# Optimization experiments

Measured on AMD Instinct MI355X. Metric: run time of the kernel, lower is better.

## Reference

```python
import jax, jax.numpy as jnp
import numpy as np

NUM_CLASSES = 2
TOP_K = 1500
CONF_THRESH = 0.01
NMS_THRESH = 0.2
VAR0, VAR1 = 0.1, 0.2  # cfg['variance']


def setup_inputs() -> dict:
    key = jax.random.key(0)
    k1, k2, k3 = jax.random.split(key, 3)
    B, P = 32, 76800
    loc_data = jax.random.normal(k1, (B, P, 4), jnp.float32)
    conf_data = jax.random.uniform(k2, (B * P, NUM_CLASSES), jnp.float32)
    prior_data = jax.random.uniform(k3, (P, 4), jnp.float32)
    return {"loc_data": loc_data, "conf_data": conf_data, "prior_data": prior_data}


def _decode(loc, priors):
    # loc, priors: [P,4]; SSD box decode with variances
    cxcy = priors[:, :2] + loc[:, :2] * VAR0 * priors[:, 2:]
    wh = priors[:, 2:] * jnp.exp(loc[:, 2:] * VAR1)
    x1y1 = cxcy - wh * 0.5
    return jnp.concatenate([x1y1, x1y1 + wh], axis=-1)  # [P,4] (x1,y1,x2,y2)


def _nms_per_class(scores, boxes):
    # scores: [P], boxes: [P,4] -> [TOP_K,5] packed (score,x1,y1,x2,y2)
    s = jnp.where(scores > CONF_THRESH, scores, -jnp.inf)
    sk, idx = jax.lax.top_k(s, TOP_K)  # torch nms keeps only top_k candidates
    bk = boxes[idx]
    x1, y1, x2, y2 = bk[:, 0], bk[:, 1], bk[:, 2], bk[:, 3]
    area = (x2 - x1) * (y2 - y1)
    iota = jnp.arange(TOP_K)

    def step(active, i):
        # greedy NMS over score-descending candidates
        xx1 = jnp.maximum(x1, x1[i]); yy1 = jnp.maximum(y1, y1[i])
        xx2 = jnp.minimum(x2, x2[i]); yy2 = jnp.minimum(y2, y2[i])
        inter = jnp.maximum(xx2 - xx1, 0.0) * jnp.maximum(yy2 - yy1, 0.0)
        iou = inter / (area + area[i] - inter)
        kept = active[i]
        suppress = (iou > NMS_THRESH) & (iota != i)
        active = jnp.where(kept, active & ~suppress, active)
        return active, kept

    _, keep = jax.lax.scan(step, sk > -jnp.inf, iota)
    rows = jnp.where(keep[:, None], jnp.concatenate([sk[:, None], bk], axis=1), 0.0)
    # pack kept rows at the front (score-descending order), zeros after
    rank = jnp.cumsum(keep) - 1
    dest = jnp.where(keep, rank, TOP_K)  # dump non-kept into scratch slot
    return jnp.zeros((TOP_K + 1, 5), bk.dtype).at[dest].set(rows)[:TOP_K]


def reference(loc_data, conf_data, prior_data):
    B, P, _ = loc_data.shape
    conf = conf_data.reshape(B, P, NUM_CLASSES)
    decoded = jax.vmap(_decode, in_axes=(0, None))(loc_data, prior_data)  # [B,P,4]
    outs = []
    for cl in range(1, NUM_CLASSES):  # background class 0 stays zero
        outs.append(jax.vmap(_nms_per_class)(conf[:, :, cl], decoded))
    bg = jnp.zeros((B, 1, TOP_K, 5), decoded.dtype)
    return jnp.concatenate([bg, jnp.stack(outs, axis=1)], axis=1)  # [B,C,TOP_K,5]
```

## Files before the change

### kernel.cpp

```cpp
#include <hip/hip_runtime.h>
#include <stdint.h>

typedef unsigned long long u64;
typedef unsigned int u32;

#define NUM_B 32
#define NUM_P 76800
#define TOPK 1500
#define NBINS 2048
#define CAP 2048
#define NWORDS 24
#define NCHUNK 6
#define HSLICES 16
#define HCHUNK (NUM_P / HSLICES)
#define PB 1984
#define SCAP 512

__device__ __forceinline__ u32 fbits(float f) { return __float_as_uint(f); }
__device__ __forceinline__ int binOf(float s) {
    int b = (int)(s * (float)NBINS);
    return (b > NBINS - 1) ? NBINS - 1 : b;
}
__device__ __forceinline__ u64 readlane64(u64 v, int l) {
    u32 lo = (u32)__builtin_amdgcn_readlane((int)(u32)(v & 0xffffffffu), l);
    u32 hi = (u32)__builtin_amdgcn_readlane((int)(u32)(v >> 32), l);
    return ((u64)hi << 32) | lo;
}

__global__ __launch_bounds__(256) void hist_kernel(const float4* __restrict__ conf4,
                                                   u32* __restrict__ hist,
                                                   u32* __restrict__ bpos,
                                                   u64* __restrict__ skey,
                                                   u32* __restrict__ scnt) {
    int c = blockIdx.x, b = blockIdx.y, tid = threadIdx.x;
    if (tid < NBINS / HSLICES) bpos[(size_t)b * NBINS + c * (NBINS / HSLICES) + tid] = 0;
    __shared__ u32 h[NBINS];
    __shared__ u64 stg[SCAP];
    __shared__ u32 sc_s;
    if (tid == 0) sc_s = 0;
    for (int i = tid; i < NBINS; i += 256) h[i] = 0;
    __syncthreads();
    const float4* base = conf4 + (size_t)b * (NUM_P / 2) + (size_t)c * (HCHUNK / 2);
    int pbase = c * HCHUNK;
    for (int i = tid; i < HCHUNK / 2; i += 256) {
        float4 v = base[i];
        int p0 = pbase + i * 2;
        if (v.y > 0.01f) {
            int bn = binOf(v.y);
            atomicAdd(&h[bn], 1u);
            if (bn >= PB) {
                u32 s = atomicAdd(&sc_s, 1u);
                if (s < SCAP) stg[s] = ((u64)fbits(v.y) << 32) | (u32)(~p0);
            }
        }
        if (v.w > 0.01f) {
            int bn = binOf(v.w);
            atomicAdd(&h[bn], 1u);
            if (bn >= PB) {
                u32 s = atomicAdd(&sc_s, 1u);
                if (s < SCAP) stg[s] = ((u64)fbits(v.w) << 32) | (u32)(~(p0 + 1));
            }
        }
    }
    __syncthreads();
    u32* outp = hist + ((size_t)b * HSLICES + c) * NBINS;
    for (int i = tid; i < NBINS; i += 256) outp[i] = h[i];
    u32 n = sc_s;
    if (tid == 0) scnt[b * HSLICES + c] = n;
    u64* sk = skey + (size_t)(b * HSLICES + c) * SCAP;
    u32 nn = (n < (u32)SCAP) ? n : (u32)SCAP;
    for (u32 i = tid; i < nn; i += 256) sk[i] = stg[i];
}

__global__ void thresh_kernel(const u32* __restrict__ hist, int* __restrict__ tbin,
                              u32* __restrict__ binbase, u32* __restrict__ bincnt,
                              u32* __restrict__ ntotal) {
    int b = blockIdx.x;
    int tid = threadIdx.x;
    int lane = tid & 63, wid = tid >> 6;
    const u32* hb = hist + (size_t)b * HSLICES * NBINS;
    __shared__ u32 wsum[4];
    __shared__ int s_min[NBINS / 256];
    if (tid < NBINS / 256) s_min[tid] = 256;
    __syncthreads();
    u32 total = 0;
    for (int c = 0; c < NBINS / 256; ++c) {
        int bin = NBINS - 1 - (c * 256 + tid);
        u32 v = 0;
#pragma unroll
        for (int s = 0; s < HSLICES; ++s) v += hb[(size_t)s * NBINS + bin];
        u32 x = v;
#pragma unroll
        for (int off = 1; off < 64; off <<= 1) {
            u32 y = __shfl_up(x, off, 64);
            if (lane >= off) x += y;
        }
        if (lane == 63) wsum[wid] = x;
        __syncthreads();
        u32 woff = 0;
        for (int w2 = 0; w2 < wid; ++w2) woff += wsum[w2];
        u32 csum = wsum[0] + wsum[1] + wsum[2] + wsum[3];
        u32 incl = woff + x;
        u32 cum = total + incl;
        binbase[(size_t)b * NBINS + bin] = cum - v;
        bincnt [(size_t)b * NBINS + bin] = v;
        if (cum >= TOPK) atomicMin(&s_min[c], tid);
        __syncthreads();
        int sm = s_min[c];
        if (sm < 256) {
            if (tid == sm) { tbin[b] = bin; ntotal[b] = cum; }
            return;
        }
        total += csum;
    }
    if (tid == 0) { tbin[b] = 0; ntotal[b] = total; }
}

__global__ __launch_bounds__(256) void compact_kernel(
    const float4* __restrict__ conf4, const int* __restrict__ tbin,
    const u32* __restrict__ binbase, u32* __restrict__ bpos,
    u64* __restrict__ keys, const u64* __restrict__ skey,
    const u32* __restrict__ scnt) {
    int b = blockIdx.y;
    int tid = threadIdx.x;
    int tb = tbin[b];
    if (tb >= PB) {
        bool ovf = false;
#pragma unroll
        for (int s = 0; s < HSLICES; ++s) ovf |= (scnt[b * HSLICES + s] > (u32)SCAP);
        if (!ovf) {
            if (blockIdx.x >= HSLICES) return;
            int sl = blockIdx.x;
            u32 cnt = scnt[b * HSLICES + sl];
            const u64* sk = skey + (size_t)(b * HSLICES + sl) * SCAP;
            for (u32 i = tid; i < cnt; i += 256) {
                u64 key = sk[i];
                float sc = __uint_as_float((u32)(key >> 32));
                int bn = binOf(sc);
                if (bn >= tb) {
                    u32 slot = atomicAdd(&bpos[(size_t)b * NBINS + bn], 1u);
                    u32 pos = binbase[(size_t)b * NBINS + bn] + slot;
                    if (pos < CAP) keys[(size_t)b * CAP + pos] = key;
                }
            }
            return;
        }
    }
    int f4 = blockIdx.x * 256 + tid;
    float4 c = conf4[(size_t)b * (NUM_P / 2) + f4];
    int p0 = f4 * 2, p1 = p0 + 1;
    int b0 = binOf(c.y);
    if (c.y > 0.01f && b0 >= tb) {
        u32 slot = atomicAdd(&bpos[(size_t)b * NBINS + b0], 1u);
        u32 pos = binbase[(size_t)b * NBINS + b0] + slot;
        if (pos < CAP) keys[(size_t)b * CAP + pos] = ((u64)fbits(c.y) << 32) | (u32)(~p0);
    }
    int b1 = binOf(c.w);
    if (c.w > 0.01f && b1 >= tb) {
        u32 slot = atomicAdd(&bpos[(size_t)b * NBINS + b1], 1u);
        u32 pos = binbase[(size_t)b * NBINS + b1] + slot;
        if (pos < CAP) keys[(size_t)b * CAP + pos] = ((u64)fbits(c.w) << 32) | (u32)(~p1);
    }
}

__global__ __launch_bounds__(256) void rank_decode_kernel(
    const u64* __restrict__ keys, const u32* __restrict__ binbase,
    const u32* __restrict__ bincnt, const u32* __restrict__ ntotal,
    const float* __restrict__ loc, const float* __restrict__ prior,
    float* __restrict__ sscore, float* __restrict__ sbox) {
#pragma clang fp contract(off)
    int b = blockIdx.y;
    int g = blockIdx.x * 256 + threadIdx.x;
    int n = (int)min(ntotal[b], (u32)CAP);
    if (g >= n) return;
    const u64* kb = keys + (size_t)b * CAP;
    u64 mykey = kb[g];
    float sc = __uint_as_float((u32)(mykey >> 32));
    int bn = binOf(sc);
    u32 start = binbase[(size_t)b * NBINS + bn];
    u32 end = start + bincnt[(size_t)b * NBINS + bn];
    if (end > (u32)n) end = (u32)n;
    u32 rank = start;
#pragma unroll 4
    for (u32 j = start; j < end; ++j) rank += (kb[j] > mykey) ? 1u : 0u;

    if (rank < TOPK) {
        u32 pidx = ~(u32)mykey;
        const float* lp = &loc[((size_t)b * NUM_P + pidx) * 4];
        const float* pp = &prior[(size_t)pidx * 4];
        float lx = lp[0], ly = lp[1], lw = lp[2], lh = lp[3];
        float pcx = pp[0], pcy = pp[1], pw = pp[2], ph = pp[3];
        float cx = pcx + (lx * 0.1f) * pw;
        float cy = pcy + (ly * 0.1f) * ph;
        float w  = pw * expf(lw * 0.2f);
        float h  = ph * expf(lh * 0.2f);
        float x1 = cx - w * 0.5f;
        float y1 = cy - h * 0.5f;
        float x2 = x1 + w;
        float y2 = y1 + h;
        sscore[(size_t)b * TOPK + rank] = sc;
        float* bx = &sbox[((size_t)b * TOPK + rank) * 4];
        bx[0] = x1; bx[1] = y1; bx[2] = x2; bx[3] = y2;
    }
}

__global__ __launch_bounds__(256) void mask_kernel(
    const float* __restrict__ sbox, u64* __restrict__ mask) {
#pragma clang fp contract(off)
    int w = blockIdx.x, c = blockIdx.y, b = blockIdx.z, tid = threadIdx.x;
    int i = c * 256 + tid;
    if ((w * 64 + 63) <= (c * 256)) return;
    __shared__ float4 cbox[64];
    __shared__ float car[64];
    if (tid < 64) {
        int j = w * 64 + tid;
        float4 bx = make_float4(0.f, 0.f, 0.f, 0.f);
        if (j < TOPK) bx = ((const float4*)sbox)[(size_t)b * TOPK + j];
        cbox[tid] = bx;
        car[tid] = (bx.z - bx.x) * (bx.w - bx.y);
    }
    __syncthreads();
    if (i < TOPK && (w * 64 + 63) > i) {
        const double MID = 0.5 * ((double)__uint_as_float(0x3E4CCCCDu) +
                                  (double)__uint_as_float(0x3E4CCCCEu));
        const float4 bx = ((const float4*)sbox)[(size_t)b * TOPK + i];
        float x1i = bx.x, y1i = bx.y, x2i = bx.z, y2i = bx.w;
        float ai = (x2i - x1i) * (y2i - y1i);
        u64 jmask = (i < w * 64) ? ~0ULL : (~0ULL << (i - w * 64 + 1));
        u64 m = 0;
        for (int j2 = 0; j2 < 64; ++j2) {
            float4 cb = cbox[j2];
            float xx1 = fmaxf(cb.x, x1i);
            float yy1 = fmaxf(cb.y, y1i);
            float xx2 = fminf(cb.z, x2i);
            float yy2 = fminf(cb.w, y2i);
            float iw = fmaxf(xx2 - xx1, 0.0f);
            float ih = fmaxf(yy2 - yy1, 0.0f);
            float inter = iw * ih;
            float denom = (car[j2] + ai) - inter;
            if ((double)inter >= MID * (double)denom) m |= (1ULL << j2);
        }
        m &= jmask;
        mask[((size_t)b * NWORDS + w) * TOPK + i] = m;
    }
}

__global__ __launch_bounds__(256) void sweep_kernel(
    const u64* __restrict__ mask, const float* __restrict__ sscore,
    const float* __restrict__ sbox, float* __restrict__ out) {
    int b = blockIdx.x, tid = threadIdx.x;
    int lane = tid & 63, wid = tid >> 6;

    const u64* mbase = mask + (size_t)b * NWORDS * TOPK;

    __shared__ u64 rowbuf[3][NWORDS][65];
    __shared__ u64 aw[NWORDS];
    __shared__ u32 pfx[NWORDS + 1];

    u64 act = 0;
    u64 sv[8];
    if (wid == 0) {
        for (int c = 0; c < NWORDS; ++c) {
            int r = c * 64 + lane;
            bool v = (r < TOPK) && (sscore[(size_t)b * TOPK + r] > 0.0f);
            u64 m = __ballot(v);
            if (lane == c) act = m;
        }
    } else {
        int w0 = (wid - 1) * 8;
#pragma unroll
        for (int t = 0; t < 2; ++t) {
            u64 tmp[8];
#pragma unroll
            for (int k = 0; k < 8; ++k)
                tmp[k] = (w0 + k >= t) ? mbase[(size_t)(w0 + k) * TOPK + t * 64 + lane] : 0ULL;
#pragma unroll
            for (int k = 0; k < 8; ++k)
                rowbuf[t][w0 + k][lane] = tmp[k];
        }
        {
            int rr = 2 * 64 + lane;
#pragma unroll
            for (int k = 0; k < 8; ++k)
                sv[k] = (w0 + k >= 2) ? mbase[(size_t)(w0 + k) * TOPK + rr] : 0ULL;
        }
    }
    __syncthreads();

    for (int T = 0; T < NWORDS; ++T) {
        if (wid == 0) {
            u64 dreg = rowbuf[T % 3][T][lane];
            u64 actw = readlane64(act, T);
            u64 kept = 0, rem = actw;
            while (rem) {
                int i2 = __ffsll(rem) - 1;
                kept |= (1ULL << i2);
                rem &= rem - 1;
                rem &= ~readlane64(dreg, i2);
            }
            if (lane == T) act = kept;
            if (lane > T && lane < NWORDS) {
                const u64* rb = rowbuf[T % 3][lane];
                if (__popcll(kept) > 4) {
                    u64 acc = 0;
#pragma unroll 16
                    for (int j = 0; j < 64; ++j) {
                        u64 sel = (u64)0 - ((kept >> j) & 1ULL);
                        acc |= rb[j] & sel;
                    }
                    act &= ~acc;
                } else {
                    u64 kb = kept;
                    while (kb) {
                        int r = __ffsll(kb) - 1;
                        kb &= kb - 1;
                        act &= ~rb[r];
                    }
                }
            }
        } else {
            int tw = T + 2;
            if (tw < NWORDS) {
                int w0 = (wid - 1) * 8;
#pragma unroll
                for (int k = 0; k < 8; ++k)
                    rowbuf[tw % 3][w0 + k][lane] = sv[k];
                int tn = T + 3;
                if (tn < NWORDS) {
                    int rr = tn * 64 + lane;
                    bool vr = rr < TOPK;
#pragma unroll
                    for (int k = 0; k < 8; ++k)
                        sv[k] = (vr && (w0 + k >= tn))
                                    ? mbase[(size_t)(w0 + k) * TOPK + rr] : 0ULL;
                }
            }
        }
        __syncthreads();
    }

    if (wid == 0 && lane < NWORDS) aw[lane] = act;
    {
        float4* pz = (float4*)(out + (size_t)b * 2 * TOPK * 5);
        float4 z4 = make_float4(0.f, 0.f, 0.f, 0.f);
        for (int t = tid; t < (2 * TOPK * 5) / 4; t += 256) pz[t] = z4;
    }
    __syncthreads();
    if (tid == 0) {
        u32 acc = 0;
        for (int wd = 0; wd < NWORDS; ++wd) { pfx[wd] = acc; acc += (u32)__popcll(aw[wd]); }
        pfx[NWORDS] = acc;
    }
    __syncthreads();
    for (int r = tid; r < TOPK; r += 256) {
        int wd = r >> 6;
        u64 word = aw[wd];
        if ((word >> (r & 63)) & 1ULL) {
            u32 rank = pfx[wd] + (u32)__popcll(word & ((1ULL << (r & 63)) - 1ULL));
            float sc = sscore[(size_t)b * TOPK + r];
            float4 bx = ((const float4*)sbox)[(size_t)b * TOPK + r];
            size_t base_o = (((size_t)b * 2 + 1) * TOPK + (size_t)rank) * 5;
            out[base_o + 0] = sc;
            out[base_o + 1] = bx.x;
            out[base_o + 2] = bx.y;
            out[base_o + 3] = bx.z;
            out[base_o + 4] = bx.w;
        }
    }
}

extern "C" void kernel_launch(void* const* d_in, const int* in_sizes, int n_in,
                              void* d_out, int out_size, void* d_ws, size_t ws_size,
                              hipStream_t stream) {
    const float* loc   = (const float*)d_in[0];
    const float* conf  = (const float*)d_in[1];
    const float* prior = (const float*)d_in[2];
    float* out = (float*)d_out;
    char* ws = (char*)d_ws;

    u64* mask_buf = (u64*)(ws + 0);
    u32* hist     = (u32*)(ws + 0);
    u32* binbase  = (u32*)(ws + 4194304);
    u32* bincnt   = (u32*)(ws + 4456448);
    u32* bpos     = (u32*)(ws + 4718592);
    u64* keys     = (u64*)(ws + 4980736);
    int* tbin     = (int*)(ws + 5505024);
    u32* ntotal   = (u32*)(ws + 5505152);
    u64* skey     = (u64*)(ws + 5505280);
    u32* scnt     = (u32*)(ws + 7602432);
    float* sscore = (float*)(ws + 9216000);
    float* sbox   = (float*)(ws + 9408000);

    hist_kernel<<<dim3(HSLICES, 32), 256, 0, stream>>>((const float4*)conf, hist, bpos,
                                                       skey, scnt);
    thresh_kernel<<<32, 256, 0, stream>>>(hist, tbin, binbase, bincnt, ntotal);
    compact_kernel<<<dim3(150, 32), 256, 0, stream>>>((const float4*)conf, tbin, binbase,
                                                      bpos, keys, skey, scnt);
    rank_decode_kernel<<<dim3(CAP / 256, 32), 256, 0, stream>>>(keys, binbase, bincnt,
                                                                ntotal, loc, prior,
                                                                sscore, sbox);
    mask_kernel<<<dim3(NWORDS, NCHUNK, 32), 256, 0, stream>>>(sbox, mask_buf);
    sweep_kernel<<<32, 256, 0, stream>>>(mask_buf, sscore, sbox, out);
}
```

Measured before the change: 182.5 us.

## Preload all upper-triangle mask tiles to LDS and drop per-step barriers in sweep

The sweep kernel used to stream mask tiles through a triple-buffered LDS ring, with a block barrier on each of the 24 word steps. It now loads every upper-triangular tile (276 pairs) into shared memory once, keeps the diagonal rows in wave-0 registers, and runs the whole greedy sweep inside wave 0 with no barriers. The other waves zero the output in parallel. The suppression OR-loop now skips 16-bit groups of kept with no bits set. The trade-off is about 143 KB of LDS per block, which limits occupancy, plus a serialized upfront load with no overlap. Wave 0 also uses 24 extra 64-bit registers.

```diff
diff --git a/kernel.cpp b/kernel.cpp
--- a/kernel.cpp
+++ b/kernel.cpp
@@ -15,6 +15,7 @@
 #define HCHUNK (NUM_P / HSLICES)
 #define PB 1984
 #define SCAP 512
+#define NPAIR 276
 
 __device__ __forceinline__ u32 fbits(float f) { return __float_as_uint(f); }
 __device__ __forceinline__ int binOf(float s) {
@@ -253,13 +254,17 @@
 
     const u64* mbase = mask + (size_t)b * NWORDS * TOPK;
 
-    __shared__ u64 rowbuf[3][NWORDS][65];
+    __shared__ u64 tb[NPAIR * 65];
     __shared__ u64 aw[NWORDS];
     __shared__ u32 pfx[NWORDS + 1];
 
     u64 act = 0;
-    u64 sv[8];
+    u64 dr[NWORDS];
+
     if (wid == 0) {
+#pragma unroll
+        for (int t = 0; t < NWORDS; ++t)
+            dr[t] = mbase[(size_t)t * TOPK + t * 64 + lane];
         for (int c = 0; c < NWORDS; ++c) {
             int r = c * 64 + lane;
             bool v = (r < TOPK) && (sscore[(size_t)b * TOPK + r] > 0.0f);
@@ -267,29 +272,18 @@
             if (lane == c) act = m;
         }
     } else {
-        int w0 = (wid - 1) * 8;
-#pragma unroll
-        for (int t = 0; t < 2; ++t) {
-            u64 tmp[8];
-#pragma unroll
-            for (int k = 0; k < 8; ++k)
-                tmp[k] = (w0 + k >= t) ? mbase[(size_t)(w0 + k) * TOPK + t * 64 + lane] : 0ULL;
-#pragma unroll
-            for (int k = 0; k < 8; ++k)
-                rowbuf[t][w0 + k][lane] = tmp[k];
-        }
-        {
-            int rr = 2 * 64 + lane;
-#pragma unroll
-            for (int k = 0; k < 8; ++k)
-                sv[k] = (w0 + k >= 2) ? mbase[(size_t)(w0 + k) * TOPK + rr] : 0ULL;
-        }
-    }
-    __syncthreads();
-
-    for (int T = 0; T < NWORDS; ++T) {
-        if (wid == 0) {
-            u64 dreg = rowbuf[T % 3][T][lane];
+        int p = 0;
+        for (int t = 0; t < NWORDS - 1; ++t)
+            for (int w = t + 1; w < NWORDS; ++w, ++p)
+                if (p % 3 == wid - 1)
+                    tb[p * 65 + lane] = mbase[(size_t)w * TOPK + t * 64 + lane];
+    }
+    __syncthreads();
+
+    if (wid == 0) {
+#pragma unroll
+        for (int T = 0; T < NWORDS; ++T) {
+            u64 dreg = dr[T];
             u64 actw = readlane64(act, T);
             u64 kept = 0, rem = actw;
             while (rem) {
@@ -300,50 +294,27 @@
             }
             if (lane == T) act = kept;
             if (lane > T && lane < NWORDS) {
-                const u64* rb = rowbuf[T % 3][lane];
-                if (__popcll(kept) > 4) {
-                    u64 acc = 0;
-#pragma unroll 16
-                    for (int j = 0; j < 64; ++j) {
-                        u64 sel = (u64)0 - ((kept >> j) & 1ULL);
-                        acc |= rb[j] & sel;
-                    }
-                    act &= ~acc;
-                } else {
-                    u64 kb = kept;
-                    while (kb) {
-                        int r = __ffsll(kb) - 1;
-                        kb &= kb - 1;
-                        act &= ~rb[r];
+                const u64* rb = &tb[((T * (47 - T)) / 2 + (lane - T - 1)) * 65];
+                u64 acc = 0;
+#pragma unroll
+                for (int b16 = 0; b16 < 4; ++b16) {
+                    if ((u32)(kept >> (b16 * 16)) & 0xffffu) {
+#pragma unroll
+                        for (int j = 0; j < 16; ++j) {
+                            int r = b16 * 16 + j;
+                            u64 sel = (u64)0 - ((kept >> r) & 1ULL);
+                            acc |= rb[r] & sel;
+                        }
                     }
                 }
-            }
-        } else {
-            int tw = T + 2;
-            if (tw < NWORDS) {
-                int w0 = (wid - 1) * 8;
-#pragma unroll
-                for (int k = 0; k < 8; ++k)
-                    rowbuf[tw % 3][w0 + k][lane] = sv[k];
-                int tn = T + 3;
-                if (tn < NWORDS) {
-                    int rr = tn * 64 + lane;
-                    bool vr = rr < TOPK;
-#pragma unroll
-                    for (int k = 0; k < 8; ++k)
-                        sv[k] = (vr && (w0 + k >= tn))
-                                    ? mbase[(size_t)(w0 + k) * TOPK + rr] : 0ULL;
-                }
-            }
-        }
-        __syncthreads();
-    }
-
-    if (wid == 0 && lane < NWORDS) aw[lane] = act;
-    {
+                act &= ~acc;
+            }
+        }
+        if (lane < NWORDS) aw[lane] = act;
+    } else {
         float4* pz = (float4*)(out + (size_t)b * 2 * TOPK * 5);
         float4 z4 = make_float4(0.f, 0.f, 0.f, 0.f);
-        for (int t = tid; t < (2 * TOPK * 5) / 4; t += 256) pz[t] = z4;
+        for (int t = tid - 64; t < (2 * TOPK * 5) / 4; t += 192) pz[t] = z4;
     }
     __syncthreads();
     if (tid == 0) {
```

Result: slower. 215.4 us (+18.0%).
